# Performance work log

Hardware: AMD Instinct MI355X
Metric: run time of the kernel (lower is better)

The kernel has to match this reference:

```python
import jax, jax.numpy as jnp
import numpy as np

B, N, D, NH, MAXLEN = 2, 2048, 1024, 16, 2048
HD = D // NH

def srel_skew(x):
    # x: [B, H, n, n] -> music-transformer skew
    b, h, n, _ = x.shape
    v = jnp.pad(x, ((0, 0), (0, 0), (0, 0), (1, 0)))  # pad last dim left
    return v.reshape(b, h, n + 1, n)[:, :, :n, :]

def split_head(x):
    # [B, n, D] -> [B, H, n, HD]
    b, n, _ = x.shape
    return x.reshape(b, n, NH, HD).transpose(0, 2, 1, 3)

def setup_inputs() -> dict:
    key = jax.random.key(0)
    ks = jax.random.split(key, 7)
    scale = 0.02
    return {
        "x": jax.random.normal(ks[0], (B, N, D), dtype=jnp.float32),
        "Wq": jax.random.normal(ks[1], (D, D), dtype=jnp.float32) * scale,
        "Wk": jax.random.normal(ks[2], (D, D), dtype=jnp.float32) * scale,
        "Wv": jax.random.normal(ks[3], (D, D), dtype=jnp.float32) * scale,
        "Wp": jax.random.normal(ks[4], (D, D), dtype=jnp.float32) * scale,
        "bp": jnp.zeros((D,), dtype=jnp.float32),
        "rel_embed": jax.random.normal(ks[5], (MAXLEN, D), dtype=jnp.float32) * scale,
    }

def reference(x, Wq, Wk, Wv, Wp, bp, rel_embed):
    b, n, d = x.shape
    qx = split_head(x @ Wq.T)  # [B,H,n,HD]
    kx = split_head(x @ Wk.T)
    vx = split_head(x @ Wv.T)
    # relative distance embeddings for last n positions
    ns = jnp.arange(n) + (MAXLEN - n)
    ex = rel_embed[ns].reshape(n, NH, HD).transpose(1, 0, 2)  # [H,n,HD]
    srel = srel_skew(jnp.einsum('bhnd,hmd->bhnm', qx, ex))  # [B,H,n,n]
    inv_dim = 1.0 / np.sqrt(d / NH)
    qk = (jnp.einsum('bhnd,bhmd->bhnm', qx, kx) + srel) * inv_dim
    mask = 1e9 * jnp.triu(jnp.ones((n, n), dtype=x.dtype), 1)
    atten = jax.nn.softmax(qk - mask, axis=-1)
    out = jnp.einsum('bhnm,bhmd->bhnd', atten, vx).transpose(0, 2, 1, 3).reshape(b, n, d)
    return out @ Wp.T + bp
```

## Files before the change

kernel.cpp:

```cpp
#include <hip/hip_runtime.h>

typedef __attribute__((ext_vector_type(8))) short short8;
typedef __attribute__((ext_vector_type(4))) short s16x4;
typedef __attribute__((ext_vector_type(4))) float f32x4;
typedef unsigned short u16t;
typedef unsigned int u32t;

#define MFMA16(a,b,c) __builtin_amdgcn_mfma_f32_16x16x32_bf16((a),(b),(c),0,0,0)

__device__ __forceinline__ f32x4 mfma16x16(s16x4 a, s16x4 b, f32x4 c) {
#if __has_builtin(__builtin_amdgcn_mfma_f32_16x16x16bf16_1k)
  return __builtin_amdgcn_mfma_f32_16x16x16bf16_1k(a, b, c, 0, 0, 0);
#else
  __asm__("v_mfma_f32_16x16x16_bf16 %0, %1, %2, %0" : "+v"(c) : "v"(a), "v"(b));
  return c;
#endif
}

constexpr int Bc = 2, Nc = 2048, Dc = 1024, NHc = 16, HDc = 64;
constexpr int EStride = Nc + 80;

__device__ __forceinline__ u16t f2bf(float f) {
  union { float f; u32t u; } v; v.f = f;
  u32t r = v.u + 0x7FFFu + ((v.u >> 16) & 1u);
  return (u16t)(r >> 16);
}
#if __has_builtin(__builtin_amdgcn_cvt_pk_bf16_f32)
__device__ __forceinline__ u32t pk2(float a, float b) {
  auto r = __builtin_amdgcn_cvt_pk_bf16_f32(a, b);
  return __builtin_bit_cast(u32t, r);
}
#else
__device__ __forceinline__ u32t pk2(float a, float b) {
  u32t ua = __builtin_bit_cast(u32t, a);
  u32t ub = __builtin_bit_cast(u32t, b);
  return ((ua + 0x8000u) >> 16) | ((ub + 0x8000u) & 0xFFFF0000u);
}
#endif
__device__ __forceinline__ s16x4 pk4(float a, float b, float c, float d) {
  union { u32t u[2]; s16x4 s; } r;
  r.u[0] = pk2(a, b); r.u[1] = pk2(c, d);
  return r.s;
}

__device__ __forceinline__ void gld16(const u16t* g, u16t* l) {
  __builtin_amdgcn_global_load_lds(
      (const __attribute__((address_space(1))) unsigned int*)(g),
      (__attribute__((address_space(3))) unsigned int*)(l), 16, 0, 0);
}

__device__ __forceinline__ void cvt4(const float* s, u16t* d) {
  f32x4 v = *(const f32x4*)s;
  u32t* dp = (u32t*)d;
  dp[0] = pk2(v[0], v[1]); dp[1] = pk2(v[2], v[3]);
}

__global__ __launch_bounds__(256) void cvt_all(
    const float* __restrict__ x, const float* __restrict__ wq,
    const float* __restrict__ wk, const float* __restrict__ wv,
    const float* __restrict__ wp, const float* __restrict__ rel,
    u16t* __restrict__ xb, u16t* __restrict__ wqb, u16t* __restrict__ wkb,
    u16t* __restrict__ wvb, u16t* __restrict__ wpb, u16t* __restrict__ Eb) {
  int i = blockIdx.x * 256 + threadIdx.x;
  if (i < 1048576) {
    cvt4(x + (size_t)i * 4, xb + (size_t)i * 4);
  } else if (i < 2097152) {
    int r = i - 1048576;
    int w = r >> 18;
    int k = (r & 262143) * 4;
    const float* s = (w == 0) ? wq : (w == 1) ? wk : (w == 2) ? wv : wp;
    u16t* d = (w == 0) ? wqb : (w == 1) ? wkb : (w == 2) ? wvb : wpb;
    cvt4(s + k, d + k);
  } else if (i < 2621440) {
    int r = i - 2097152;
    int flat = r * 4;
    int h = flat >> 17;
    int rem = flat & 131071;
    int m = rem >> 6, d = rem & 63;
    cvt4(rel + (size_t)m * Dc + h * HDc + d,
         Eb + ((size_t)h * EStride + m) * HDc + d);
  } else {
    int r = i - 2621440;
    int flat = r * 4;
    int h = flat / 5120;
    int rem = flat - h * 5120;
    int pr = rem >> 6, d = rem & 63;
    u32t* dp = (u32t*)(Eb + ((size_t)h * EStride + Nc + pr) * HDc + d);
    dp[0] = 0; dp[1] = 0;
  }
}

__global__ __launch_bounds__(256, 3) void gemm_qkv(const u16t* __restrict__ A,
    const u16t* __restrict__ Wq, const u16t* __restrict__ Wk,
    const u16t* __restrict__ Wv, u16t* __restrict__ Qb,
    u16t* __restrict__ Kb, u16t* __restrict__ Vt) {
  __shared__ u16t lA[128 * 32];
  __shared__ u16t lB[128 * 32];
  const int y = blockIdx.y, which = y >> 3;
  const u16t* W = (which == 0) ? Wq : (which == 1) ? Wk : Wv;
  const float sc = (which == 0) ? 0.18033688011112042f : 1.0f;
  const int m0 = blockIdx.x * 128, n0 = (y & 7) * 128;
  const int t = threadIdx.x, wave = t >> 6, lane = t & 63;
  const int l15 = lane & 15, q4 = lane >> 4, wm = wave & 1, wn = wave >> 1;
  const int srow = wave * 16 + (lane >> 2);
  const int scol = (lane & 3) * 8;

  f32x4 acc[4][4];
  for (int i = 0; i < 4; i++)
    for (int j = 0; j < 4; j++)
      for (int r = 0; r < 4; r++) acc[i][j][r] = 0.f;

  for (int k0 = 0; k0 < Dc; k0 += 32) {
    __syncthreads();
    for (int r = 0; r < 2; r++) {
      int row = srow + r * 64;
      gld16(A + (size_t)(m0 + row) * Dc + k0 + scol, lA + wave * 512 + r * 2048);
      gld16(W + (size_t)(n0 + row) * Dc + k0 + scol, lB + wave * 512 + r * 2048);
    }
    __syncthreads();
    short8 af[4], bf[4];
    for (int i = 0; i < 4; i++) {
      af[i] = *(const short8*)(&lA[(wm * 64 + i * 16 + l15) * 32 + q4 * 8]);
      bf[i] = *(const short8*)(&lB[(wn * 64 + i * 16 + l15) * 32 + q4 * 8]);
    }
    for (int mi = 0; mi < 4; mi++)
      for (int ni = 0; ni < 4; ni++)
        acc[mi][ni] = MFMA16(af[mi], bf[ni], acc[mi][ni]);
  }

  if (which < 2) {
    for (int mi = 0; mi < 4; mi++)
      for (int ni = 0; ni < 4; ni++)
        for (int rg = 0; rg < 4; rg++) {
          int gm = m0 + wm * 64 + mi * 16 + q4 * 4 + rg;
          int gn = n0 + wn * 64 + ni * 16 + l15;
          int b = gm >> 11, n = gm & 2047, h = gn >> 6, hd = gn & 63;
          u16t* outb = (which == 0) ? Qb : Kb;
          outb[(((size_t)(b * NHc + h) * Nc + n) * HDc) + hd] =
              f2bf(acc[mi][ni][rg] * sc);
        }
  } else {
    for (int mi = 0; mi < 4; mi++)
      for (int ni = 0; ni < 4; ni++) {
        int gm = m0 + wm * 64 + mi * 16 + q4 * 4;
        int gn = n0 + wn * 64 + ni * 16 + l15;
        int b = gm >> 11, n = gm & 2047, h = gn >> 6, hd = gn & 63;
        s16x4 pkv = pk4(acc[mi][ni][0], acc[mi][ni][1],
                        acc[mi][ni][2], acc[mi][ni][3]);
        *(s16x4*)(&Vt[((size_t)(b * NHc + h) * HDc + hd) * Nc + n]) = pkv;
      }
  }
}

__global__ __launch_bounds__(256, 2) void gemm_proj(const u16t* __restrict__ A,
    const u16t* __restrict__ W, float* __restrict__ outf,
    const float* __restrict__ bias) {
  __shared__ u16t lA[64 * 32];
  __shared__ u16t lB[128 * 32];
  const int m0 = blockIdx.x * 64, n0 = blockIdx.y * 128;
  const int t = threadIdx.x, wave = t >> 6, lane = t & 63;
  const int l15 = lane & 15, q4 = lane >> 4, wm = wave & 1, wn = wave >> 1;
  const int srow = wave * 16 + (lane >> 2);
  const int scol = (lane & 3) * 8;

  f32x4 acc[2][4];
  for (int i = 0; i < 2; i++)
    for (int j = 0; j < 4; j++)
      for (int r = 0; r < 4; r++) acc[i][j][r] = 0.f;

  for (int k0 = 0; k0 < Dc; k0 += 32) {
    __syncthreads();
    gld16(A + (size_t)(m0 + srow) * Dc + k0 + scol, lA + wave * 512);
    for (int r = 0; r < 2; r++) {
      int row = srow + r * 64;
      gld16(W + (size_t)(n0 + row) * Dc + k0 + scol, lB + wave * 512 + r * 2048);
    }
    __syncthreads();
    short8 af[2], bf[4];
    for (int i = 0; i < 2; i++)
      af[i] = *(const short8*)(&lA[(wm * 32 + i * 16 + l15) * 32 + q4 * 8]);
    for (int i = 0; i < 4; i++)
      bf[i] = *(const short8*)(&lB[(wn * 64 + i * 16 + l15) * 32 + q4 * 8]);
    for (int mi = 0; mi < 2; mi++)
      for (int ni = 0; ni < 4; ni++)
        acc[mi][ni] = MFMA16(af[mi], bf[ni], acc[mi][ni]);
  }

  for (int mi = 0; mi < 2; mi++)
    for (int ni = 0; ni < 4; ni++)
      for (int rg = 0; rg < 4; rg++) {
        int gm = m0 + wm * 32 + mi * 16 + q4 * 4 + rg;
        int gn = n0 + wn * 64 + ni * 16 + l15;
        outf[(size_t)gm * Dc + gn] = acc[mi][ni][rg] + bias[gn];
      }
}

__global__ __launch_bounds__(256, 2) void attn(const u16t* __restrict__ Qb,
                                               const u16t* __restrict__ Kb,
                                               const u16t* __restrict__ Vt,
                                               const u16t* __restrict__ Eb,
                                               u16t* __restrict__ AO) {
  __shared__ u16t lK[64 * 72];
  __shared__ u16t lE[128 * 72];
  __shared__ u16t lV[64 * 72];
  __shared__ float Ps[4][16 * 84];

  const int xbk = blockIdx.x;
  const int h = blockIdx.y, b = blockIdx.z;
  const u16t* Qh = Qb + (size_t)(b * NHc + h) * Nc * HDc;
  const u16t* Kh = Kb + (size_t)(b * NHc + h) * Nc * HDc;
  const u16t* Vh = Vt + (size_t)(b * NHc + h) * HDc * Nc;
  const u16t* Eh = Eb + (size_t)h * EStride * HDc;

  const int t = threadIdx.x, wave = t >> 6, lane = t & 63, l15 = lane & 15, q4 = lane >> 4;
  const int tbase = (3 - wave) * 16;
  const int Tm = wave * 16 + l15;
  float* Pw = Ps[wave];

  const int sr = t >> 3, sc8 = (t & 7) * 8;
  const int sr2 = sr + 32;

  for (int ph = 0; ph < 2; ph++) {
    const int qi = ph ? xbk : (31 - xbk);
    const int r0 = qi * 64;
    const int rw = r0 + wave * 16;

    short8 qf[2], qsf[2];
    {
      int r = rw + l15;
      int rs = r - 1; if (rs < 0) rs = 0;
      for (int kh = 0; kh < 2; kh++) {
        qf[kh]  = *(const short8*)(Qh + (size_t)r * HDc + kh * 32 + q4 * 8);
        qsf[kh] = *(const short8*)(Qh + (size_t)rs * HDc + kh * 32 + q4 * 8);
      }
    }

    f32x4 accO[4];
    float l_p = 0.f;
    for (int dt = 0; dt < 4; dt++)
      for (int rg = 0; rg < 4; rg++) accO[dt][rg] = 0.f;

    auto body = [&](int j, bool last) {
      f32x4 accS[4];
      for (int ct = 0; ct < 4; ct++)
        for (int rg = 0; rg < 4; rg++) accS[ct][rg] = 0.f;
      for (int kh = 0; kh < 2; kh++)
        for (int ct = 0; ct < 4; ct++) {
          short8 kfr = *(const short8*)(&lK[(ct * 16 + l15) * 72 + kh * 32 + q4 * 8]);
          accS[ct] = MFMA16(kfr, qf[kh], accS[ct]);
        }
      const int rot = (j & 1) << 6;
      f32x4 accP[5];
      for (int pt = 0; pt < 5; pt++)
        for (int rg = 0; rg < 4; rg++) accP[pt][rg] = 0.f;
      for (int kh = 0; kh < 2; kh++)
        for (int pt = 0; pt < 5; pt++) {
          int prow = (tbase + pt * 16 + l15 + rot) & 127;
          short8 efr = *(const short8*)(&lE[prow * 72 + kh * 32 + q4 * 8]);
          accP[pt] = MFMA16(efr, qsf[kh], accP[pt]);
        }
      for (int pt = 0; pt < 5; pt++)
        *(f32x4*)(&Pw[l15 * 84 + pt * 16 + q4 * 4]) = accP[pt];
      __asm__ volatile("s_waitcnt lgkmcnt(0)" ::: "memory");
      const int rbase = l15 * 83 + q4 * 4 + 15;
      float pv[4][4];
      for (int ct = 0; ct < 4; ct++)
        for (int rg = 0; rg < 4; rg++) {
          float s = accS[ct][rg] + Pw[rbase + ct * 16 + rg];
          if (last && (ct * 16 + q4 * 4 + rg) > Tm) s = -1e30f;
          float p = exp2f(s);
          l_p += p;
          pv[ct][rg] = p;
        }
      __asm__ volatile("" ::: "memory");
      s16x4 bq[4];
      for (int ks = 0; ks < 4; ks++)
        bq[ks] = pk4(pv[ks][0], pv[ks][1], pv[ks][2], pv[ks][3]);
      for (int dt = 0; dt < 4; dt++)
        for (int ks = 0; ks < 4; ks++) {
          s16x4 vfr = *(const s16x4*)(&lV[(dt * 16 + l15) * 72 + ks * 16 + q4 * 4]);
          accO[dt] = mfma16x16(vfr, bq[ks], accO[dt]);
        }
    };

    {
      *(f32x4*)(&lK[sr * 72 + sc8])  = *(const f32x4*)(Kh + (size_t)sr * HDc + sc8);
      *(f32x4*)(&lK[sr2 * 72 + sc8]) = *(const f32x4*)(Kh + (size_t)sr2 * HDc + sc8);
      *(f32x4*)(&lV[sr * 72 + sc8])  = *(const f32x4*)(Vh + (size_t)sr * Nc + sc8);
      *(f32x4*)(&lV[sr2 * 72 + sc8]) = *(const f32x4*)(Vh + (size_t)sr2 * Nc + sc8);
      const int ebase0 = Nc - 63 - r0;
      for (int i = 0; i < 4; i++) {
        int cc = t + i * 256;
        int s = cc >> 3, c8 = (cc & 7) * 8;
        *(f32x4*)(&lE[s * 72 + c8]) =
            *(const f32x4*)(Eh + (size_t)(ebase0 + s) * HDc + c8);
      }
    }

    for (int j = 0; j < qi; j++) {
      __syncthreads();
      const int cn = j * 64 + 64;
      f32x4 pK0 = *(const f32x4*)(Kh + (size_t)(cn + sr) * HDc + sc8);
      f32x4 pK1 = *(const f32x4*)(Kh + (size_t)(cn + sr2) * HDc + sc8);
      f32x4 pV0 = *(const f32x4*)(Vh + (size_t)sr * Nc + cn + sc8);
      f32x4 pV1 = *(const f32x4*)(Vh + (size_t)sr2 * Nc + cn + sc8);
      const int ebn = 64 * (j + 1) - r0 + (Nc - 63) + 64;
      f32x4 pE0 = *(const f32x4*)(Eh + (size_t)(ebn + sr) * HDc + sc8);
      f32x4 pE1 = *(const f32x4*)(Eh + (size_t)(ebn + sr2) * HDc + sc8);

      body(j, false);

      __syncthreads();
      *(f32x4*)(&lK[sr * 72 + sc8])  = pK0;
      *(f32x4*)(&lK[sr2 * 72 + sc8]) = pK1;
      *(f32x4*)(&lV[sr * 72 + sc8])  = pV0;
      *(f32x4*)(&lV[sr2 * 72 + sc8]) = pV1;
      int ph0 = (sr + 64 * j) & 127;
      int ph1 = (sr2 + 64 * j) & 127;
      *(f32x4*)(&lE[ph0 * 72 + sc8]) = pE0;
      *(f32x4*)(&lE[ph1 * 72 + sc8]) = pE1;
    }

    __syncthreads();
    body(qi, true);

    float l2 = l_p + __shfl_xor(l_p, 16);
    float lt = l2 + __shfl_xor(l2, 32);
    float inv = 1.f / lt;
    {
      int r = rw + l15;
      u16t* dst = AO + (size_t)(b * Nc + r) * Dc + h * HDc + q4 * 4;
      for (int dt = 0; dt < 4; dt++) {
        s16x4 o = pk4(accO[dt][0] * inv, accO[dt][1] * inv,
                      accO[dt][2] * inv, accO[dt][3] * inv);
        *(s16x4*)(dst + dt * 16) = o;
      }
    }
  }
}

extern "C" void kernel_launch(void* const* d_in, const int* in_sizes, int n_in,
                              void* d_out, int out_size, void* d_ws, size_t ws_size,
                              hipStream_t stream) {
  (void)in_sizes; (void)n_in; (void)out_size; (void)ws_size;
  const float* x   = (const float*)d_in[0];
  const float* Wq  = (const float*)d_in[1];
  const float* Wk  = (const float*)d_in[2];
  const float* Wv  = (const float*)d_in[3];
  const float* Wp  = (const float*)d_in[4];
  const float* bp  = (const float*)d_in[5];
  const float* rel = (const float*)d_in[6];
  float* out = (float*)d_out;

  char* ws = (char*)d_ws;
  u16t* xb  = (u16t*)(ws);
  u16t* wqb = (u16t*)(ws + 8388608);
  u16t* wkb = (u16t*)(ws + 10485760);
  u16t* wvb = (u16t*)(ws + 12582912);
  u16t* wpb = (u16t*)(ws + 14680064);
  u16t* Eb  = (u16t*)(ws + 16777216);
  u16t* Qb  = (u16t*)(ws + 21233664);
  u16t* Kb  = (u16t*)(ws + 29622272);
  u16t* Vtb = (u16t*)(ws + 38010880);
  u16t* AOb = (u16t*)(ws + 46399488);

  cvt_all<<<10320, 256, 0, stream>>>(x, Wq, Wk, Wv, Wp, rel,
                                     xb, wqb, wkb, wvb, wpb, Eb);
  gemm_qkv<<<dim3(32, 24), 256, 0, stream>>>(xb, wqb, wkb, wvb, Qb, Kb, Vtb);
  attn<<<dim3(16, NHc, Bc), 256, 0, stream>>>(Qb, Kb, Vtb, Eb, AOb);
  gemm_proj<<<dim3(64, 8), 256, 0, stream>>>(AOb, wpb, out, bp);
}
```

Measured before the change: 213.7 us.

## Store K and V in MFMA fragment order and load them directly into registers

The QKV GEMM epilogue now writes K and V into a tiled layout that matches the per-lane MFMA operand order, 4096 elements per 64-key block. The attention kernel then loads K and V fragments straight from global memory into registers instead of staging them through LDS, which removes the lK/lV buffers and their shared-memory writes and reads. The relative-position product is also computed before QK^T. The risks are less coalesced scatter writes in the GEMM epilogue, global-load latency that is no longer hidden by prefetching, and higher register pressure from holding 16 short8 fragments. The K scale also changes: K is now stored unscaled and sc is applied unconditionally, which only matters on the Q path.

After: 213.9 us. About the same (+0.1%).

```diff
diff --git a/kernel.cpp b/kernel.cpp
--- a/kernel.cpp
+++ b/kernel.cpp
@@ -41,6 +41,13 @@
   union { u32t u[2]; s16x4 s; } r;
   r.u[0] = pk2(a, b); r.u[1] = pk2(c, d);
   return r.s;
+}
+
+__device__ __forceinline__ s16x4 lo4(short8 v) {
+  return __builtin_shufflevector(v, v, 0, 1, 2, 3);
+}
+__device__ __forceinline__ s16x4 hi4(short8 v) {
+  return __builtin_shufflevector(v, v, 4, 5, 6, 7);
 }
 
 __device__ __forceinline__ void gld16(const u16t* g, u16t* l) {
@@ -98,7 +105,7 @@
   __shared__ u16t lB[128 * 32];
   const int y = blockIdx.y, which = y >> 3;
   const u16t* W = (which == 0) ? Wq : (which == 1) ? Wk : Wv;
-  const float sc = (which == 0) ? 0.18033688011112042f : 1.0f;
+  const float sc = 0.18033688011112042f;
   const int m0 = blockIdx.x * 128, n0 = (y & 7) * 128;
   const int t = threadIdx.x, wave = t >> 6, lane = t & 63;
   const int l15 = lane & 15, q4 = lane >> 4, wm = wave & 1, wn = wave >> 1;
@@ -128,16 +135,28 @@
         acc[mi][ni] = MFMA16(af[mi], bf[ni], acc[mi][ni]);
   }
 
-  if (which < 2) {
+  if (which == 0) {
     for (int mi = 0; mi < 4; mi++)
       for (int ni = 0; ni < 4; ni++)
         for (int rg = 0; rg < 4; rg++) {
           int gm = m0 + wm * 64 + mi * 16 + q4 * 4 + rg;
           int gn = n0 + wn * 64 + ni * 16 + l15;
           int b = gm >> 11, n = gm & 2047, h = gn >> 6, hd = gn & 63;
-          u16t* outb = (which == 0) ? Qb : Kb;
-          outb[(((size_t)(b * NHc + h) * Nc + n) * HDc) + hd] =
+          Qb[(((size_t)(b * NHc + h) * Nc + n) * HDc) + hd] =
               f2bf(acc[mi][ni][rg] * sc);
+        }
+  } else if (which == 1) {
+    for (int mi = 0; mi < 4; mi++)
+      for (int ni = 0; ni < 4; ni++)
+        for (int rg = 0; rg < 4; rg++) {
+          int gm = m0 + wm * 64 + mi * 16 + q4 * 4 + rg;
+          int gn = n0 + wn * 64 + ni * 16 + l15;
+          int b = gm >> 11, n = gm & 2047, h = gn >> 6, hd = gn & 63;
+          size_t off = (size_t)(b * NHc + h) * Nc * HDc
+                     + (size_t)(n >> 6) * 4096
+                     + ((((n >> 4) & 3) * 2 + (hd >> 5)) * 512)
+                     + (((hd >> 3) & 3) * 128) + ((n & 15) * 8) + (hd & 7);
+          Kb[off] = f2bf(acc[mi][ni][rg]);
         }
   } else {
     for (int mi = 0; mi < 4; mi++)
@@ -147,7 +166,12 @@
         int b = gm >> 11, n = gm & 2047, h = gn >> 6, hd = gn & 63;
         s16x4 pkv = pk4(acc[mi][ni][0], acc[mi][ni][1],
                         acc[mi][ni][2], acc[mi][ni][3]);
-        *(s16x4*)(&Vt[((size_t)(b * NHc + h) * HDc + hd) * Nc + n]) = pkv;
+        size_t off = (size_t)(b * NHc + h) * Nc * HDc
+                   + (size_t)(n >> 6) * 4096
+                   + (((hd >> 4) * 2 + ((n >> 5) & 1)) * 512)
+                   + (((n >> 2) & 3) * 128) + ((hd & 15) * 8)
+                   + (((n >> 4) & 1) * 4);
+        *(s16x4*)(&Vt[off]) = pkv;
       }
   }
 }
@@ -200,16 +224,14 @@
                                                const u16t* __restrict__ Vt,
                                                const u16t* __restrict__ Eb,
                                                u16t* __restrict__ AO) {
-  __shared__ u16t lK[64 * 72];
   __shared__ u16t lE[128 * 72];
-  __shared__ u16t lV[64 * 72];
   __shared__ float Ps[4][16 * 84];
 
   const int xbk = blockIdx.x;
   const int h = blockIdx.y, b = blockIdx.z;
   const u16t* Qh = Qb + (size_t)(b * NHc + h) * Nc * HDc;
   const u16t* Kh = Kb + (size_t)(b * NHc + h) * Nc * HDc;
-  const u16t* Vh = Vt + (size_t)(b * NHc + h) * HDc * Nc;
+  const u16t* Vh = Vt + (size_t)(b * NHc + h) * Nc * HDc;
   const u16t* Eh = Eb + (size_t)h * EStride * HDc;
 
   const int t = threadIdx.x, wave = t >> 6, lane = t & 63, l15 = lane & 15, q4 = lane >> 4;
@@ -241,26 +263,39 @@
       for (int rg = 0; rg < 4; rg++) accO[dt][rg] = 0.f;
 
     auto body = [&](int j, bool last) {
+      const u16t* Kt = Kh + (size_t)j * 4096;
+      const u16t* Vj = Vh + (size_t)j * 4096;
+      short8 kf[8], vf[8];
+#pragma unroll
+      for (int i = 0; i < 8; i++)
+        kf[i] = *(const short8*)(Kt + i * 512 + lane * 8);
+#pragma unroll
+      for (int i = 0; i < 8; i++)
+        vf[i] = *(const short8*)(Vj + i * 512 + lane * 8);
+
+      const int rot = (j & 1) << 6;
+      const int pbase = tbase + l15 + rot;
+#pragma unroll
+      for (int pt = 0; pt < 5; pt++) {
+        f32x4 ap;
+        ap[0] = 0.f; ap[1] = 0.f; ap[2] = 0.f; ap[3] = 0.f;
+#pragma unroll
+        for (int kh = 0; kh < 2; kh++) {
+          int prow = (pbase + pt * 16) & 127;
+          short8 efr = *(const short8*)(&lE[prow * 72 + kh * 32 + q4 * 8]);
+          ap = MFMA16(efr, qsf[kh], ap);
+        }
+        *(f32x4*)(&Pw[l15 * 84 + pt * 16 + q4 * 4]) = ap;
+      }
       f32x4 accS[4];
       for (int ct = 0; ct < 4; ct++)
         for (int rg = 0; rg < 4; rg++) accS[ct][rg] = 0.f;
+#pragma unroll
       for (int kh = 0; kh < 2; kh++)
-        for (int ct = 0; ct < 4; ct++) {
-          short8 kfr = *(const short8*)(&lK[(ct * 16 + l15) * 72 + kh * 32 + q4 * 8]);
-          accS[ct] = MFMA16(kfr, qf[kh], accS[ct]);
-        }
-      const int rot = (j & 1) << 6;
-      f32x4 accP[5];
-      for (int pt = 0; pt < 5; pt++)
-        for (int rg = 0; rg < 4; rg++) accP[pt][rg] = 0.f;
-      for (int kh = 0; kh < 2; kh++)
-        for (int pt = 0; pt < 5; pt++) {
-          int prow = (tbase + pt * 16 + l15 + rot) & 127;
-          short8 efr = *(const short8*)(&lE[prow * 72 + kh * 32 + q4 * 8]);
-          accP[pt] = MFMA16(efr, qsf[kh], accP[pt]);
-        }
-      for (int pt = 0; pt < 5; pt++)
-        *(f32x4*)(&Pw[l15 * 84 + pt * 16 + q4 * 4]) = accP[pt];
+#pragma unroll
+        for (int ct = 0; ct < 4; ct++)
+          accS[ct] = MFMA16(kf[ct * 2 + kh], qf[kh], accS[ct]);
+
       __asm__ volatile("s_waitcnt lgkmcnt(0)" ::: "memory");
       const int rbase = l15 * 83 + q4 * 4 + 15;
       float pv[4][4];
@@ -276,18 +311,18 @@
       s16x4 bq[4];
       for (int ks = 0; ks < 4; ks++)
         bq[ks] = pk4(pv[ks][0], pv[ks][1], pv[ks][2], pv[ks][3]);
+#pragma unroll
       for (int dt = 0; dt < 4; dt++)
+#pragma unroll
         for (int ks = 0; ks < 4; ks++) {
-          s16x4 vfr = *(const s16x4*)(&lV[(dt * 16 + l15) * 72 + ks * 16 + q4 * 4]);
+          s16x4 vfr = (ks & 1) ? hi4(vf[dt * 2 + (ks >> 1)])
+                               : lo4(vf[dt * 2 + (ks >> 1)]);
           accO[dt] = mfma16x16(vfr, bq[ks], accO[dt]);
         }
     };
 
+    __syncthreads();
     {
-      *(f32x4*)(&lK[sr * 72 + sc8])  = *(const f32x4*)(Kh + (size_t)sr * HDc + sc8);
-      *(f32x4*)(&lK[sr2 * 72 + sc8]) = *(const f32x4*)(Kh + (size_t)sr2 * HDc + sc8);
-      *(f32x4*)(&lV[sr * 72 + sc8])  = *(const f32x4*)(Vh + (size_t)sr * Nc + sc8);
-      *(f32x4*)(&lV[sr2 * 72 + sc8]) = *(const f32x4*)(Vh + (size_t)sr2 * Nc + sc8);
       const int ebase0 = Nc - 63 - r0;
       for (int i = 0; i < 4; i++) {
         int cc = t + i * 256;
@@ -299,11 +334,6 @@
 
     for (int j = 0; j < qi; j++) {
       __syncthreads();
-      const int cn = j * 64 + 64;
-      f32x4 pK0 = *(const f32x4*)(Kh + (size_t)(cn + sr) * HDc + sc8);
-      f32x4 pK1 = *(const f32x4*)(Kh + (size_t)(cn + sr2) * HDc + sc8);
-      f32x4 pV0 = *(const f32x4*)(Vh + (size_t)sr * Nc + cn + sc8);
-      f32x4 pV1 = *(const f32x4*)(Vh + (size_t)sr2 * Nc + cn + sc8);
       const int ebn = 64 * (j + 1) - r0 + (Nc - 63) + 64;
       f32x4 pE0 = *(const f32x4*)(Eh + (size_t)(ebn + sr) * HDc + sc8);
       f32x4 pE1 = *(const f32x4*)(Eh + (size_t)(ebn + sr2) * HDc + sc8);
@@ -311,10 +341,6 @@
       body(j, false);
 
       __syncthreads();
-      *(f32x4*)(&lK[sr * 72 + sc8])  = pK0;
-      *(f32x4*)(&lK[sr2 * 72 + sc8]) = pK1;
-      *(f32x4*)(&lV[sr * 72 + sc8])  = pV0;
-      *(f32x4*)(&lV[sr2 * 72 + sc8]) = pV1;
       int ph0 = (sr + 64 * j) & 127;
       int ph1 = (sr2 + 64 * j) & 127;
       *(f32x4*)(&lE[ph0 * 72 + sc8]) = pE0;
```
